# Kernel tuning notes

Hardware: AMD Instinct MI355X
Metric: run time of the kernel (lower is better)

## Reference

```python
import jax, jax.numpy as jnp
import numpy as np

N_NODES = 10000
N_EDGES = 320000
FEAT = 256


def setup_inputs() -> dict:
    key = jax.random.key(0)
    k1, k2, k3 = jax.random.split(key, 3)
    src = jax.random.normal(k1, (N_EDGES, FEAT), dtype=jnp.float32)
    edge_index = jax.random.randint(k2, (2, N_EDGES), 0, N_NODES, dtype=jnp.int64)
    W = jax.random.normal(k3, (FEAT, FEAT), dtype=jnp.float32) / np.sqrt(FEAT)
    b = jnp.zeros((FEAT,), dtype=jnp.float32)
    return {
        "source_node_representation_with_coefficient": src,
        "edge_index": edge_index,
        "feature_dim": FEAT,
        "W": W,
        "b": b,
    }


def reference(source_node_representation_with_coefficient, edge_index, feature_dim, W, b):
    dst = edge_index[1]  # [E] destination node of each edge
    # scatter_mean over dim 0: segment sum / segment count (0 for empty segments)
    seg_sum = jax.ops.segment_sum(
        source_node_representation_with_coefficient, dst, num_segments=N_NODES
    )  # [N, F]
    counts = jax.ops.segment_sum(
        jnp.ones((dst.shape[0],), dtype=source_node_representation_with_coefficient.dtype),
        dst,
        num_segments=N_NODES,
    )  # [N]
    denom = jnp.maximum(counts, 1.0)[:, None]
    aggregated = jnp.where(counts[:, None] > 0, seg_sum / denom, 0.0)  # [N, F]
    # Linear(feature_dim, feature_dim): y = x @ W.T + b
    return aggregated @ W.T + b
```

## Files before the change

kernel.cpp:

```cpp
#include <hip/hip_runtime.h>

#define N_NODES 10000
#define N_EDGES 320000
#define FEAT    256
#define NB      16
#define CAP     128

__global__ __launch_bounds__(256) void fill1_kernel(
    const int* __restrict__ dst, int* __restrict__ curs, int* __restrict__ bucket)
{
    const int e = blockIdx.x * 256 + threadIdx.x;
    if (e < N_EDGES) {
        const int n   = dst[e];
        const int pos = atomicAdd(&curs[n], 1);
        if (pos < CAP) bucket[(n << 7) + pos] = e;
    }
}

__global__ __launch_bounds__(256) void gather_kernel(
    const float* __restrict__ src,
    const int*   __restrict__ curs,
    const int*   __restrict__ bucket,
    float*       __restrict__ out_mean)
{
    const int t    = threadIdx.x;
    const int lane = t & 63;
    const int w    = t >> 6;
    const int n    = (blockIdx.x << 2) + w;
    if (n >= N_NODES) return;

    const int deg = curs[n];
    const int dc  = min(deg, CAP);
    const int sbase = n << 7;
    const size_t foff = (size_t)(lane << 2);

    float4 acc[8];
    #pragma unroll
    for (int j = 0; j < 8; ++j) acc[j] = make_float4(0.f, 0.f, 0.f, 0.f);

    for (int base = 0; base < dc; base += 64) {
        const int m = min(64, dc - base);
        const int eidx = bucket[sbase + base + min(lane, m - 1)];

        for (int k = 0; k < m; k += 8) {
            int   e[8];
            float s[8];
            #pragma unroll
            for (int j = 0; j < 8; ++j) {
                const int kk = min(k + j, m - 1);
                e[j] = __shfl(eidx, kk);
                s[j] = (k + j < m) ? 1.0f : 0.0f;
            }
            float4 v[8];
            #pragma unroll
            for (int j = 0; j < 8; ++j) {
                v[j] = *reinterpret_cast<const float4*>(
                    src + (size_t)e[j] * FEAT + foff);
            }
            #pragma unroll
            for (int j = 0; j < 8; ++j) {
                acc[j].x = fmaf(v[j].x, s[j], acc[j].x);
                acc[j].y = fmaf(v[j].y, s[j], acc[j].y);
                acc[j].z = fmaf(v[j].z, s[j], acc[j].z);
                acc[j].w = fmaf(v[j].w, s[j], acc[j].w);
            }
        }
    }

    float4 r = make_float4(0.f, 0.f, 0.f, 0.f);
    #pragma unroll
    for (int j = 0; j < 8; ++j) {
        r.x += acc[j].x; r.y += acc[j].y; r.z += acc[j].z; r.w += acc[j].w;
    }

    const float inv = (deg > 0) ? 1.0f / (float)deg : 0.0f;
    r.x *= inv; r.y *= inv; r.z *= inv; r.w *= inv;
    *reinterpret_cast<float4*>(out_mean + (size_t)n * FEAT + foff) = r;
}

__global__ __launch_bounds__(256) void linear_kernel(
    const float* x,
    const float* __restrict__ W,
    const float* __restrict__ bias,
    float*       y)
{
    __shared__ float s_rows[NB][FEAT];
    const int t  = threadIdx.x;
    const int n0 = blockIdx.x * NB;

    #pragma unroll
    for (int n = 0; n < NB; ++n) {
        const int node = n0 + n;
        s_rows[n][t] = (node < N_NODES) ? x[(size_t)node * FEAT + t] : 0.f;
    }
    __syncthreads();

    float acc[NB];
    #pragma unroll
    for (int n = 0; n < NB; ++n) acc[n] = 0.0f;

    const float* wrow = W + (size_t)t * FEAT;
    for (int f = 0; f < FEAT; f += 4) {
        const float4 w4 = *reinterpret_cast<const float4*>(wrow + f);
        #pragma unroll
        for (int n = 0; n < NB; ++n) {
            const float4 s4 = *reinterpret_cast<const float4*>(&s_rows[n][f]);
            acc[n] = fmaf(s4.x, w4.x, acc[n]);
            acc[n] = fmaf(s4.y, w4.y, acc[n]);
            acc[n] = fmaf(s4.z, w4.z, acc[n]);
            acc[n] = fmaf(s4.w, w4.w, acc[n]);
        }
    }

    const float bj = bias[t];
    #pragma unroll
    for (int n = 0; n < NB; ++n) {
        const int node = n0 + n;
        if (node < N_NODES) y[(size_t)node * FEAT + t] = acc[n] + bj;
    }
}

extern "C" void kernel_launch(void* const* d_in, const int* in_sizes, int n_in,
                              void* d_out, int out_size, void* d_ws, size_t ws_size,
                              hipStream_t stream)
{
    const float* src = (const float*)d_in[0];
    const int*   ei  = (const int*)d_in[1];
    const int*   dst = ei + N_EDGES;
    const float* W   = (const float*)d_in[3];
    const float* b   = (const float*)d_in[4];
    float*       out = (float*)d_out;

    int* curs   = (int*)d_ws;
    int* bucket = curs + 10240;

    hipMemsetAsync(curs, 0, N_NODES * sizeof(int), stream);

    fill1_kernel<<<(N_EDGES + 255) / 256, 256, 0, stream>>>(dst, curs, bucket);

    gather_kernel<<<(N_NODES + 3) / 4, 256, 0, stream>>>(src, curs, bucket, out);
    linear_kernel<<<(N_NODES + NB - 1) / NB, 256, 0, stream>>>(out, W, b, out);
}
```

Before: 141.2 us.

## Fuse mean aggregation and linear layer into one kernel via shared memory

Merges the gather/mean kernel and the linear kernel into a single kernel. Each block computes the means for 4 nodes into shared memory, then applies W and the bias directly. This removes a kernel launch and the round trip of the intermediate mean matrix through global memory. In exchange each block now reads the full W for only 4 nodes instead of 16, so reads of W, mostly served from cache, grow fourfold. The bounds checks are dropped because the grid divides N_NODES exactly.

```diff
diff --git a/kernel.cpp b/kernel.cpp
--- a/kernel.cpp
+++ b/kernel.cpp
@@ -3,7 +3,6 @@
 #define N_NODES 10000
 #define N_EDGES 320000
 #define FEAT    256
-#define NB      16
 #define CAP     128
 
 __global__ __launch_bounds__(256) void fill1_kernel(
@@ -17,106 +16,94 @@
     }
 }
 
-__global__ __launch_bounds__(256) void gather_kernel(
+__global__ __launch_bounds__(256) void fused_kernel(
     const float* __restrict__ src,
     const int*   __restrict__ curs,
     const int*   __restrict__ bucket,
-    float*       __restrict__ out_mean)
+    const float* __restrict__ W,
+    const float* __restrict__ bias,
+    float*       __restrict__ out)
 {
+    __shared__ float s_mean[4][FEAT];
+
     const int t    = threadIdx.x;
     const int lane = t & 63;
     const int w    = t >> 6;
     const int n    = (blockIdx.x << 2) + w;
-    if (n >= N_NODES) return;
 
-    const int deg = curs[n];
-    const int dc  = min(deg, CAP);
-    const int sbase = n << 7;
-    const size_t foff = (size_t)(lane << 2);
+    {
+        const int deg   = curs[n];
+        const int dc    = min(deg, CAP);
+        const int sbase = n << 7;
+        const size_t foff = (size_t)(lane << 2);
 
-    float4 acc[8];
-    #pragma unroll
-    for (int j = 0; j < 8; ++j) acc[j] = make_float4(0.f, 0.f, 0.f, 0.f);
+        float4 acc[8];
+        #pragma unroll
+        for (int j = 0; j < 8; ++j) acc[j] = make_float4(0.f, 0.f, 0.f, 0.f);
 
-    for (int base = 0; base < dc; base += 64) {
-        const int m = min(64, dc - base);
-        const int eidx = bucket[sbase + base + min(lane, m - 1)];
+        for (int base = 0; base < dc; base += 64) {
+            const int m = min(64, dc - base);
+            const int eidx = bucket[sbase + base + min(lane, m - 1)];
 
-        for (int k = 0; k < m; k += 8) {
-            int   e[8];
-            float s[8];
-            #pragma unroll
-            for (int j = 0; j < 8; ++j) {
-                const int kk = min(k + j, m - 1);
-                e[j] = __shfl(eidx, kk);
-                s[j] = (k + j < m) ? 1.0f : 0.0f;
-            }
-            float4 v[8];
-            #pragma unroll
-            for (int j = 0; j < 8; ++j) {
-                v[j] = *reinterpret_cast<const float4*>(
-                    src + (size_t)e[j] * FEAT + foff);
-            }
-            #pragma unroll
-            for (int j = 0; j < 8; ++j) {
-                acc[j].x = fmaf(v[j].x, s[j], acc[j].x);
-                acc[j].y = fmaf(v[j].y, s[j], acc[j].y);
-                acc[j].z = fmaf(v[j].z, s[j], acc[j].z);
-                acc[j].w = fmaf(v[j].w, s[j], acc[j].w);
+            for (int k = 0; k < m; k += 8) {
+                int   e[8];
+                float s[8];
+                #pragma unroll
+                for (int j = 0; j < 8; ++j) {
+                    const int kk = min(k + j, m - 1);
+                    e[j] = __shfl(eidx, kk);
+                    s[j] = (k + j < m) ? 1.0f : 0.0f;
+                }
+                float4 v[8];
+                #pragma unroll
+                for (int j = 0; j < 8; ++j) {
+                    v[j] = *reinterpret_cast<const float4*>(
+                        src + (size_t)e[j] * FEAT + foff);
+                }
+                #pragma unroll
+                for (int j = 0; j < 8; ++j) {
+                    acc[j].x = fmaf(v[j].x, s[j], acc[j].x);
+                    acc[j].y = fmaf(v[j].y, s[j], acc[j].y);
+                    acc[j].z = fmaf(v[j].z, s[j], acc[j].z);
+                    acc[j].w = fmaf(v[j].w, s[j], acc[j].w);
+                }
             }
         }
-    }
 
-    float4 r = make_float4(0.f, 0.f, 0.f, 0.f);
-    #pragma unroll
-    for (int j = 0; j < 8; ++j) {
-        r.x += acc[j].x; r.y += acc[j].y; r.z += acc[j].z; r.w += acc[j].w;
-    }
+        float4 r = make_float4(0.f, 0.f, 0.f, 0.f);
+        #pragma unroll
+        for (int j = 0; j < 8; ++j) {
+            r.x += acc[j].x; r.y += acc[j].y; r.z += acc[j].z; r.w += acc[j].w;
+        }
 
-    const float inv = (deg > 0) ? 1.0f / (float)deg : 0.0f;
-    r.x *= inv; r.y *= inv; r.z *= inv; r.w *= inv;
-    *reinterpret_cast<float4*>(out_mean + (size_t)n * FEAT + foff) = r;
-}
-
-__global__ __launch_bounds__(256) void linear_kernel(
-    const float* x,
-    const float* __restrict__ W,
-    const float* __restrict__ bias,
-    float*       y)
-{
-    __shared__ float s_rows[NB][FEAT];
-    const int t  = threadIdx.x;
-    const int n0 = blockIdx.x * NB;
-
-    #pragma unroll
-    for (int n = 0; n < NB; ++n) {
-        const int node = n0 + n;
-        s_rows[n][t] = (node < N_NODES) ? x[(size_t)node * FEAT + t] : 0.f;
+        const float inv = (deg > 0) ? 1.0f / (float)deg : 0.0f;
+        r.x *= inv; r.y *= inv; r.z *= inv; r.w *= inv;
+        *reinterpret_cast<float4*>(&s_mean[w][lane << 2]) = r;
     }
     __syncthreads();
 
-    float acc[NB];
-    #pragma unroll
-    for (int n = 0; n < NB; ++n) acc[n] = 0.0f;
+    {
+        const int n0 = blockIdx.x << 2;
+        float lacc[4] = {0.f, 0.f, 0.f, 0.f};
 
-    const float* wrow = W + (size_t)t * FEAT;
-    for (int f = 0; f < FEAT; f += 4) {
-        const float4 w4 = *reinterpret_cast<const float4*>(wrow + f);
+        const float* wrow = W + (size_t)t * FEAT;
+        for (int f = 0; f < FEAT; f += 4) {
+            const float4 w4 = *reinterpret_cast<const float4*>(wrow + f);
+            #pragma unroll
+            for (int nn = 0; nn < 4; ++nn) {
+                const float4 m4 = *reinterpret_cast<const float4*>(&s_mean[nn][f]);
+                lacc[nn] = fmaf(m4.x, w4.x, lacc[nn]);
+                lacc[nn] = fmaf(m4.y, w4.y, lacc[nn]);
+                lacc[nn] = fmaf(m4.z, w4.z, lacc[nn]);
+                lacc[nn] = fmaf(m4.w, w4.w, lacc[nn]);
+            }
+        }
+
+        const float bj = bias[t];
         #pragma unroll
-        for (int n = 0; n < NB; ++n) {
-            const float4 s4 = *reinterpret_cast<const float4*>(&s_rows[n][f]);
-            acc[n] = fmaf(s4.x, w4.x, acc[n]);
-            acc[n] = fmaf(s4.y, w4.y, acc[n]);
-            acc[n] = fmaf(s4.z, w4.z, acc[n]);
-            acc[n] = fmaf(s4.w, w4.w, acc[n]);
+        for (int nn = 0; nn < 4; ++nn) {
+            out[(size_t)(n0 + nn) * FEAT + t] = lacc[nn] + bj;
         }
-    }
-
-    const float bj = bias[t];
-    #pragma unroll
-    for (int n = 0; n < NB; ++n) {
-        const int node = n0 + n;
-        if (node < N_NODES) y[(size_t)node * FEAT + t] = acc[n] + bj;
     }
 }
 
@@ -138,6 +125,5 @@
 
     fill1_kernel<<<(N_EDGES + 255) / 256, 256, 0, stream>>>(dst, curs, bucket);
 
-    gather_kernel<<<(N_NODES + 3) / 4, 256, 0, stream>>>(src, curs, bucket, out);
-    linear_kernel<<<(N_NODES + NB - 1) / NB, 256, 0, stream>>>(out, W, b, out);
+    fused_kernel<<<N_NODES / 4, 256, 0, stream>>>(src, curs, bucket, W, b, out);
 }
```

Measured after the change: 168.6 us. 1.19x slower.
